# Performance work log

Hardware: AMD Instinct MI355X
Metric: run time of the kernel (lower is better)

Reference implementation:

```python
import jax, jax.numpy as jnp
import numpy as np

K = 4
KS = 7
SHIFT = KS // 2

def setup_inputs() -> dict:
    key = jax.random.key(0)
    ks = jax.random.split(key, 5)
    B, C, H, W = 8, 128, 256, 256
    x = jax.random.normal(ks[0], (B, C, H, W), dtype=jnp.float32)
    guidance = jax.random.normal(ks[1], (B, C, H, W), dtype=jnp.float32)
    basis_filters = jax.random.normal(ks[2], (K, C, KS, KS), dtype=jnp.float32)
    w1 = jax.random.normal(ks[3], (C // 4, C), dtype=jnp.float32) * (1.0 / np.sqrt(C))
    b1 = jnp.zeros((C // 4,), dtype=jnp.float32)
    w2 = jax.random.normal(ks[4], (K, C // 4), dtype=jnp.float32) * (1.0 / np.sqrt(C // 4))
    b2 = jnp.zeros((K,), dtype=jnp.float32)
    return {"x": x, "guidance": guidance, "basis_filters": basis_filters,
            "w1": w1, "b1": b1, "w2": w2, "b2": b2}

def reference(x, guidance, basis_filters, w1, b1, w2, b2):
    B, C, H, W = x.shape
    # guidance vector: global average pool -> MLP -> softmax over k bases
    g = jnp.mean(guidance, axis=(2, 3))                      # [B, C]
    h1 = jax.nn.relu(g @ w1.T + b1)                          # [B, C//4]
    weights = jax.nn.softmax(h1 @ w2.T + b2, axis=1)         # [B, K]
    # dynamic per-sample depthwise kernel: weighted sum of bases
    dyn = jnp.einsum('bk,kcij->bcij', weights, basis_filters)  # [B, C, KS, KS]
    # pad kernel to full (H, W) at the bottom/right, then roll to center at origin
    padded = jnp.pad(dyn, ((0, 0), (0, 0), (0, H - KS), (0, W - KS)))
    centered = jnp.roll(padded, shift=(-SHIFT, -SHIFT), axis=(-2, -1))
    # circular depthwise convolution via FFT
    filt_fft = jnp.fft.rfft2(centered, s=(H, W), axes=(-2, -1))
    x_fft = jnp.fft.rfft2(x, s=(H, W), axes=(-2, -1))
    out = jnp.fft.irfft2(x_fft * filt_fft, s=(H, W), axes=(-2, -1))
    return out
```

## Files before the change

### kernel.cpp

```cpp
#include <hip/hip_runtime.h>

#define HW 256
#define HWMASK 255
#define CH 128
#define BATCH 8
#define NK 4
#define STRIP 16
#define NIN (STRIP + 6)

typedef float f32x4 __attribute__((ext_vector_type(4)));

__global__ __launch_bounds__(256) void mean1_kernel(const float* __restrict__ guid,
                                                    float* __restrict__ partial) {
    int blk = blockIdx.x;
    const float4* p = (const float4*)(guid + (size_t)blk * 16384);
    float s = 0.f;
    for (int i = threadIdx.x; i < 4096; i += 256) {
        float4 v = p[i];
        s += (v.x + v.y) + (v.z + v.w);
    }
    for (int off = 32; off; off >>= 1) s += __shfl_down(s, off, 64);
    __shared__ float red[4];
    if ((threadIdx.x & 63) == 0) red[threadIdx.x >> 6] = s;
    __syncthreads();
    if (threadIdx.x == 0) partial[blk] = (red[0] + red[1]) + (red[2] + red[3]);
}

__global__ __launch_bounds__(256) void mlp_kernel(const float* __restrict__ partial,
                                                  const float* __restrict__ w1,
                                                  const float* __restrict__ b1,
                                                  const float* __restrict__ w2,
                                                  const float* __restrict__ b2,
                                                  float* __restrict__ wt) {
    __shared__ float gs[BATCH * CH];
    __shared__ float h1[BATCH * 32];
    __shared__ float lg[BATCH * NK];
    int t = threadIdx.x;
    for (int i = t; i < BATCH * CH; i += 256) {
        float4 v = *(const float4*)(partial + i * 4);
        gs[i] = ((v.x + v.y) + (v.z + v.w)) * (1.0f / 65536.0f);
    }
    __syncthreads();
    {
        int b = t >> 5, j = t & 31;
        float acc = b1[j];
        #pragma unroll 4
        for (int c = 0; c < CH; ++c) acc += gs[b * CH + c] * w1[j * CH + c];
        h1[b * 32 + j] = fmaxf(acc, 0.f);
    }
    __syncthreads();
    if (t < BATCH * NK) {
        int b = t >> 2, k = t & 3;
        float acc = b2[k];
        #pragma unroll
        for (int j = 0; j < 32; ++j) acc += h1[b * 32 + j] * w2[k * 32 + j];
        lg[b * NK + k] = acc;
    }
    __syncthreads();
    if (t < BATCH) {
        int b = t;
        float m = lg[b * 4];
        for (int k = 1; k < 4; ++k) m = fmaxf(m, lg[b * 4 + k]);
        float e[4], s = 0.f;
        for (int k = 0; k < 4; ++k) { e[k] = expf(lg[b * 4 + k] - m); s += e[k]; }
        float inv = 1.0f / s;
        for (int k = 0; k < 4; ++k) wt[b * 4 + k] = e[k] * inv;
    }
}

__global__ __launch_bounds__(256) void dyn_kernel(const float* __restrict__ wt,
                                                  const float* __restrict__ basis,
                                                  float* __restrict__ dynF) {
    int idx = blockIdx.x * 256 + threadIdx.x;
    if (idx >= BATCH * CH * 49) return;
    int ij = idx % 49;
    int bc = idx / 49;
    int c = bc % CH;
    int b = bc / CH;
    float acc = 0.f;
    #pragma unroll
    for (int k = 0; k < NK; ++k)
        acc += wt[b * NK + k] * basis[(k * CH + c) * 49 + ij];
    dynF[bc * 49 + (48 - ij)] = acc;
}

__global__ __launch_bounds__(256) void conv_kernel(const float* __restrict__ x,
                                                   const float* __restrict__ dynF,
                                                   float* __restrict__ out) {
    int bc = blockIdx.x;
    const float* xp = x + (size_t)bc * (HW * HW);
    float* op = out + (size_t)bc * (HW * HW);
    int tid = threadIdx.x;
    int lane = tid & 63, ty = tid >> 6;
    int yb = blockIdx.y * (4 * STRIP) + ty * STRIP;

    const float* df = dynF + bc * 49;
    float d[49];
    #pragma unroll
    for (int i = 0; i < 49; ++i) d[i] = df[i];

    int col = 4 * lane;
    int lL = (lane + 63) & 63;
    int lR = (lane + 1) & 63;

    float4 pf[4];
    #pragma unroll
    for (int k = 0; k < 4; ++k)
        pf[k] = *(const float4*)(xp + (((yb + k - 3) & HWMASK) * HW) + col);

    float acc[7][4] = {};
    #pragma unroll
    for (int i = 0; i < NIN; ++i) {
        float4 Q = pf[i & 3];
        if (i + 4 < NIN)
            pf[i & 3] = *(const float4*)(xp + (((yb + i + 1) & HWMASK) * HW) + col);

        float4 L, R;
        L.x = __shfl(Q.x, lL, 64); L.y = __shfl(Q.y, lL, 64);
        L.z = __shfl(Q.z, lL, 64); L.w = __shfl(Q.w, lL, 64);
        R.x = __shfl(Q.x, lR, 64); R.y = __shfl(Q.y, lR, 64);
        R.z = __shfl(Q.z, lR, 64); R.w = __shfl(Q.w, lR, 64);
        float v[12] = {L.x, L.y, L.z, L.w, Q.x, Q.y, Q.z, Q.w, R.x, R.y, R.z, R.w};

        #pragma unroll
        for (int ii = 0; ii < 7; ++ii) {
            int o = i - ii;
            if (o >= 0 && o < STRIP) {
                const int s = ((unsigned)o) % 7;
                #pragma unroll
                for (int q = 0; q < 4; ++q) {
                    #pragma unroll
                    for (int jj = 0; jj < 7; ++jj)
                        acc[s][q] += d[ii * 7 + jj] * v[q + jj + 1];
                }
            }
        }
        if (i >= 6) {
            const int o = i - 6;
            const int s = ((unsigned)o) % 7;
            f32x4 ov = {acc[s][0], acc[s][1], acc[s][2], acc[s][3]};
            __builtin_nontemporal_store(ov, (f32x4*)(op + (yb + o) * HW + col));
            acc[s][0] = 0.f; acc[s][1] = 0.f; acc[s][2] = 0.f; acc[s][3] = 0.f;
        }
    }
}

extern "C" void kernel_launch(void* const* d_in, const int* in_sizes, int n_in,
                              void* d_out, int out_size, void* d_ws, size_t ws_size,
                              hipStream_t stream) {
    const float* x        = (const float*)d_in[0];
    const float* guidance = (const float*)d_in[1];
    const float* basis    = (const float*)d_in[2];
    const float* w1       = (const float*)d_in[3];
    const float* b1       = (const float*)d_in[4];
    const float* w2       = (const float*)d_in[5];
    const float* b2       = (const float*)d_in[6];
    float* out = (float*)d_out;
    float* ws  = (float*)d_ws;

    float* partial = ws;
    float* wt      = ws + 4096;
    float* dynF    = ws + 4096 + 32;

    mean1_kernel<<<4096, 256, 0, stream>>>(guidance, partial);
    mlp_kernel<<<1, 256, 0, stream>>>(partial, w1, b1, w2, b2, wt);
    dyn_kernel<<<(BATCH * CH * 49 + 255) / 256, 256, 0, stream>>>(wt, basis, dynF);
    conv_kernel<<<dim3(BATCH * CH, HW / (4 * STRIP)), 256, 0, stream>>>(x, dynF, out);
}
```

Measured before the change: 171.0 us.

## Process 64-row strips per wave with rolling 7-row register window in conv

The conv kernel now has each wave cover 64 output rows, so one block handles a whole 256x256 plane and the grid drops its y dimension. A 7-entry register ring of prefetched rows feeds a loop of period 7, which keeps the accumulator slot indices compile-time constants. This cuts the 6-row halo reloads per strip from 6/16 to 6/64 of the input. In exchange the grid shrinks from 4096 to 1024 blocks and each wave's serial work grows, which lowers parallelism and may change register pressure.

New measurement: 177.5 us. 3.8% more time.

```diff
diff --git a/kernel.cpp b/kernel.cpp
--- a/kernel.cpp
+++ b/kernel.cpp
@@ -5,8 +5,6 @@
 #define CH 128
 #define BATCH 8
 #define NK 4
-#define STRIP 16
-#define NIN (STRIP + 6)
 
 typedef float f32x4 __attribute__((ext_vector_type(4)));
 
@@ -92,7 +90,7 @@
     float* op = out + (size_t)bc * (HW * HW);
     int tid = threadIdx.x;
     int lane = tid & 63, ty = tid >> 6;
-    int yb = blockIdx.y * (4 * STRIP) + ty * STRIP;
+    int yb = ty * 64;
 
     const float* df = dynF + bc * 49;
     float d[49];
@@ -103,46 +101,54 @@
     int lL = (lane + 63) & 63;
     int lR = (lane + 1) & 63;
 
-    float4 pf[4];
+    float4 pf[7];
     #pragma unroll
-    for (int k = 0; k < 4; ++k)
-        pf[k] = *(const float4*)(xp + (((yb + k - 3) & HWMASK) * HW) + col);
+    for (int p = 0; p < 7; ++p)
+        pf[p] = *(const float4*)(xp + (((yb + p - 3) & HWMASK) * HW) + col);
 
     float acc[7][4] = {};
+
+    #define ROWBODY(P, IIMAX, PREFROW, DOPREF, DOSTORE, OROW)                          \
+        {                                                                              \
+            float4 Q = pf[P];                                                          \
+            if (DOPREF)                                                                \
+                pf[P] = *(const float4*)(xp + (((PREFROW) & HWMASK) * HW) + col);      \
+            float4 L, R;                                                               \
+            L.x = __shfl(Q.x, lL, 64); L.y = __shfl(Q.y, lL, 64);                      \
+            L.z = __shfl(Q.z, lL, 64); L.w = __shfl(Q.w, lL, 64);                      \
+            R.x = __shfl(Q.x, lR, 64); R.y = __shfl(Q.y, lR, 64);                      \
+            R.z = __shfl(Q.z, lR, 64); R.w = __shfl(Q.w, lR, 64);                      \
+            float v[12] = {L.x, L.y, L.z, L.w, Q.x, Q.y, Q.z, Q.w, R.x, R.y, R.z, R.w};\
+            _Pragma("unroll")                                                          \
+            for (int ii = 0; ii <= (IIMAX); ++ii) {                                    \
+                const int s = ((P) - ii + 7) % 7;                                      \
+                _Pragma("unroll")                                                      \
+                for (int q = 0; q < 4; ++q) {                                          \
+                    _Pragma("unroll")                                                  \
+                    for (int jj = 0; jj < 7; ++jj)                                     \
+                        acc[s][q] += d[ii * 7 + jj] * v[q + jj + 1];                   \
+                }                                                                      \
+            }                                                                          \
+            if (DOSTORE) {                                                             \
+                const int s = ((P) + 1) % 7;                                           \
+                f32x4 ov = {acc[s][0], acc[s][1], acc[s][2], acc[s][3]};               \
+                __builtin_nontemporal_store(ov, (f32x4*)(op + (OROW) * HW + col));     \
+                acc[s][0] = 0.f; acc[s][1] = 0.f; acc[s][2] = 0.f; acc[s][3] = 0.f;    \
+            }                                                                          \
+        }
+
     #pragma unroll
-    for (int i = 0; i < NIN; ++i) {
-        float4 Q = pf[i & 3];
-        if (i + 4 < NIN)
-            pf[i & 3] = *(const float4*)(xp + (((yb + i + 1) & HWMASK) * HW) + col);
+    for (int p = 0; p < 7; ++p)
+        ROWBODY(p, p, yb + 4 + p, 1, p == 6, yb);
 
-        float4 L, R;
-        L.x = __shfl(Q.x, lL, 64); L.y = __shfl(Q.y, lL, 64);
-        L.z = __shfl(Q.z, lL, 64); L.w = __shfl(Q.w, lL, 64);
-        R.x = __shfl(Q.x, lR, 64); R.y = __shfl(Q.y, lR, 64);
-        R.z = __shfl(Q.z, lR, 64); R.w = __shfl(Q.w, lR, 64);
-        float v[12] = {L.x, L.y, L.z, L.w, Q.x, Q.y, Q.z, Q.w, R.x, R.y, R.z, R.w};
-
+    #pragma unroll 1
+    for (int g = 1; g < 10; ++g) {
+        int rowa = yb - 3 + 7 * g;
         #pragma unroll
-        for (int ii = 0; ii < 7; ++ii) {
-            int o = i - ii;
-            if (o >= 0 && o < STRIP) {
-                const int s = ((unsigned)o) % 7;
-                #pragma unroll
-                for (int q = 0; q < 4; ++q) {
-                    #pragma unroll
-                    for (int jj = 0; jj < 7; ++jj)
-                        acc[s][q] += d[ii * 7 + jj] * v[q + jj + 1];
-                }
-            }
-        }
-        if (i >= 6) {
-            const int o = i - 6;
-            const int s = ((unsigned)o) % 7;
-            f32x4 ov = {acc[s][0], acc[s][1], acc[s][2], acc[s][3]};
-            __builtin_nontemporal_store(ov, (f32x4*)(op + (yb + o) * HW + col));
-            acc[s][0] = 0.f; acc[s][1] = 0.f; acc[s][2] = 0.f; acc[s][3] = 0.f;
-        }
+        for (int p = 0; p < 7; ++p)
+            ROWBODY(p, 6, rowa + 7 + p, g < 9, 1, yb + 7 * g + p - 6);
     }
+    #undef ROWBODY
 }
 
 extern "C" void kernel_launch(void* const* d_in, const int* in_sizes, int n_in,
@@ -159,11 +165,11 @@
     float* ws  = (float*)d_ws;
 
     float* partial = ws;
-    float* wt      = ws + 4096;
+    float* wtb     = ws + 4096;
     float* dynF    = ws + 4096 + 32;
 
     mean1_kernel<<<4096, 256, 0, stream>>>(guidance, partial);
-    mlp_kernel<<<1, 256, 0, stream>>>(partial, w1, b1, w2, b2, wt);
-    dyn_kernel<<<(BATCH * CH * 49 + 255) / 256, 256, 0, stream>>>(wt, basis, dynF);
-    conv_kernel<<<dim3(BATCH * CH, HW / (4 * STRIP)), 256, 0, stream>>>(x, dynF, out);
+    mlp_kernel<<<1, 256, 0, stream>>>(partial, w1, b1, w2, b2, wtb);
+    dyn_kernel<<<(BATCH * CH * 49 + 255) / 256, 256, 0, stream>>>(wtb, basis, dynF);
+    conv_kernel<<<BATCH * CH, 256, 0, stream>>>(x, dynF, out);
 }
```
